# Performance work log

Hardware: AMD Instinct MI355X
Metric: run time of the kernel (lower is better)

## Reference

```python
import jax, jax.numpy as jnp
import numpy as np
import math

B, C, H, W = 4, 256, 64, 64
E = 96  # embed_dim
SOFTMAX_SCALE = 10.0
RESIDUAL_SCALE_INIT = 0.1


def conv1x1(w, x):
    # w: [out_c, in_c], x: [b, in_c, h, w] -> [b, out_c, h, w]
    return jnp.einsum('oc,bchw->bohw', w, x)


def setup_inputs() -> dict:
    key = jax.random.key(0)
    ks = jax.random.split(key, 12)
    s = 0.02
    return {
        'x': jax.random.normal(ks[0], (B, C, H, W), jnp.float32),
        'mask': jax.random.uniform(ks[1], (B, 1, H, W), jnp.float32),
        'ln_gamma': jnp.ones((C,), jnp.float32),
        'ln_beta': jnp.zeros((C,), jnp.float32),
        'wq': jax.random.normal(ks[2], (E, C), jnp.float32) * s,
        'wk': jax.random.normal(ks[3], (E, C), jnp.float32) * s,
        'wv': jax.random.normal(ks[4], (C, C), jnp.float32) * s,
        'w_out': jax.random.normal(ks[5], (C, C), jnp.float32) * s,
        'w_qm': jax.random.normal(ks[6], (E, 1), jnp.float32) * s,
        'wd1': jax.random.normal(ks[7], (C, 2 * C), jnp.float32) * s,
        'wd2': jax.random.normal(ks[8], (C, C), jnp.float32) * s,
        'wg': jax.random.normal(ks[9], (C, C + 1), jnp.float32) * s,
        'residual_scale': jnp.asarray(RESIDUAL_SCALE_INIT, jnp.float32),
    }


def reference(x, mask, ln_gamma, ln_beta, wq, wk, wv, w_out, w_qm, wd1, wd2, wg,
              residual_scale):
    b, c, h, w = x.shape
    n = h * w

    # ChannelLayerNorm: LayerNorm over channel dim
    mu = jnp.mean(x, axis=1, keepdims=True)
    var = jnp.mean((x - mu) ** 2, axis=1, keepdims=True)
    x_norm = (x - mu) / jnp.sqrt(var + 1e-5)
    x_norm = x_norm * ln_gamma[None, :, None, None] + ln_beta[None, :, None, None]

    # Q/K/V projections (1x1 convs), flatten to [b, n, d]
    q = conv1x1(wq, x_norm) + conv1x1(w_qm, mask)
    q = q.reshape(b, E, n).transpose(0, 2, 1)        # [b, n, E]
    k = conv1x1(wk, x_norm).reshape(b, E, n).transpose(0, 2, 1)  # [b, n, E]
    v = conv1x1(wv, x).reshape(b, c, n).transpose(0, 2, 1)       # [b, n, C]

    # cosine normalization (F.normalize with eps=1e-12)
    q = q / jnp.clip(jnp.linalg.norm(q, axis=-1, keepdims=True), 1e-12)
    k = k / jnp.clip(jnp.linalg.norm(k, axis=-1, keepdims=True), 1e-12)

    scale = SOFTMAX_SCALE / math.sqrt(E)
    attn = jnp.einsum('bqe,bke->bqk', q, k) * scale  # [b, n, n]

    # keys with mask >= 0.5 are invalid -> bias -10000
    invalid_keys = (mask.reshape(b, 1, n) >= 0.5)    # [b, 1, n]
    attn = jnp.where(invalid_keys, jnp.float32(-10000.0), attn)
    attn = jax.nn.softmax(attn, axis=-1)

    attended = jnp.einsum('bqk,bkc->bqc', attn, v)   # [b, n, C]
    attended = attended.transpose(0, 2, 1).reshape(b, c, h, w)
    attended = conv1x1(w_out, attended)

    # delta correction branch
    corr_in = jnp.concatenate([attended - x, x_norm * mask], axis=1)  # [b, 2C, h, w]
    hidden = jax.nn.gelu(conv1x1(wd1, corr_in), approximate=False)
    corrective = conv1x1(wd2, hidden)

    # MaskConditionedGate (assumed): sigmoid(1x1 conv over [corrective, mask])
    gate_in = jnp.concatenate([corrective, mask], axis=1)  # [b, C+1, h, w]
    gate = jax.nn.sigmoid(conv1x1(wg, gate_in)) * mask

    delta = jnp.tanh(residual_scale) * gate * corrective
    return x + delta
```

## Files before the change

### kernel.cpp

```cpp
#include <hip/hip_runtime.h>
#include <hip/hip_bf16.h>
#include <math.h>

#define BB 4
#define CC 256
#define NN 4096
#define EE 96
#define NTOT (BB*NN)

typedef __attribute__((ext_vector_type(8))) short bf16x8;
typedef __attribute__((ext_vector_type(4))) float f32x4;

__device__ __forceinline__ short f2bf(float x) {
    __hip_bfloat16 h = __float2bfloat16(x);
    return *reinterpret_cast<short*>(&h);
}
__device__ __forceinline__ float bf2f(short s) {
    unsigned int u = ((unsigned int)(unsigned short)s) << 16;
    float f;
    __builtin_memcpy(&f, &u, 4);
    return f;
}
__device__ __forceinline__ float gelu_exact(float v) {
    return 0.5f * v * (1.0f + erff(v * 0.70710678118654752f));
}
__device__ __forceinline__ void gld16(void* lds, const void* g) {
    __builtin_amdgcn_global_load_lds(
        (const __attribute__((address_space(1))) unsigned int*)g,
        (__attribute__((address_space(3))) unsigned int*)lds, 16, 0, 0);
}

#define OFF_WQ  0
#define OFF_WK  24576
#define OFF_WV  49152
#define OFF_WO  114688
#define OFF_WD1 180224
#define OFF_WD2 311296
#define OFF_WG  376832
#define OFF_WGL 442368
#define W16_TOTAL 442624

__global__ void wconv_kernel(const float* __restrict__ wq, const float* __restrict__ wk,
                             const float* __restrict__ wv, const float* __restrict__ wo,
                             const float* __restrict__ wd1, const float* __restrict__ wd2,
                             const float* __restrict__ wg, short* __restrict__ W16) {
    int i = blockIdx.x * 256 + threadIdx.x;
    if (i >= W16_TOTAL) return;
    float v;
    if      (i < OFF_WK)  v = wq[i];
    else if (i < OFF_WV)  v = wk[i - OFF_WK];
    else if (i < OFF_WO)  v = wv[i - OFF_WV];
    else if (i < OFF_WD1) v = wo[i - OFF_WO];
    else if (i < OFF_WD2) v = wd1[i - OFF_WD1];
    else if (i < OFF_WG)  v = wd2[i - OFF_WD2];
    else if (i < OFF_WGL) { int l = i - OFF_WG; v = wg[(l >> 8) * 257 + (l & 255)]; }
    else                  v = wg[(i - OFF_WGL) * 257 + 256];
    W16[i] = f2bf(v);
}

__global__ __launch_bounds__(256) void ln_kernel(
    const float* __restrict__ x, const float* __restrict__ gamma,
    const float* __restrict__ beta,
    short* __restrict__ Xt16, short* __restrict__ Xn16) {
    __shared__ float tile[256 * 33];
    __shared__ float psum[8][32], psq[8][32];
    __shared__ float mu_s[32], rs_s[32];
    __shared__ float gs[256], bs[256];
    const int b  = blockIdx.x >> 7;
    const int p0 = (blockIdx.x & 127) * 32;
    const int tid = threadIdx.x;
    const float* xb = x + (size_t)b * CC * NN;

    gs[tid] = gamma[tid];
    bs[tid] = beta[tid];
    #pragma unroll
    for (int i = 0; i < 8; ++i) {
        int idx = tid + i * 256;
        int c = idx >> 3, p4 = (idx & 7) * 4;
        float4 v = *(const float4*)&xb[(size_t)c * NN + p0 + p4];
        tile[c * 33 + p4]     = v.x;
        tile[c * 33 + p4 + 1] = v.y;
        tile[c * 33 + p4 + 2] = v.z;
        tile[c * 33 + p4 + 3] = v.w;
    }
    __syncthreads();
    {
        int col = tid & 31, part = tid >> 5;
        float s = 0.f, sq = 0.f;
        for (int r = part * 32; r < part * 32 + 32; ++r) {
            float v = tile[r * 33 + col];
            s += v; sq += v * v;
        }
        psum[part][col] = s; psq[part][col] = sq;
    }
    __syncthreads();
    if (tid < 32) {
        float S = 0.f, SQ = 0.f;
        #pragma unroll
        for (int j = 0; j < 8; ++j) { S += psum[j][tid]; SQ += psq[j][tid]; }
        float mu = S / 256.0f;
        float var = SQ / 256.0f - mu * mu;
        mu_s[tid] = mu;
        rs_s[tid] = rsqrtf(var + 1e-5f);
    }
    __syncthreads();
    size_t rowbase = ((size_t)b * NN + p0) * CC;
    #pragma unroll
    for (int i = 0; i < 4; ++i) {
        int idx = tid + i * 256;
        int p = idx >> 5, c8 = (idx & 31) * 8;
        float mu = mu_s[p], rcp = rs_s[p];
        bf16x8 xt, xn;
        #pragma unroll
        for (int j = 0; j < 8; ++j) {
            float v = tile[(c8 + j) * 33 + p];
            float n = (v - mu) * rcp * gs[c8 + j] + bs[c8 + j];
            xt[j] = f2bf(v); xn[j] = f2bf(n);
        }
        size_t o = rowbase + (size_t)p * CC + c8;
        *(bf16x8*)&Xt16[o] = xt;
        *(bf16x8*)&Xn16[o] = xn;
    }
}

__global__ __launch_bounds__(256) void qkproj_kernel(
    const short* __restrict__ Xn16, const short* __restrict__ W16,
    const float* __restrict__ mask, const float* __restrict__ w_qm,
    short* __restrict__ Q16, short* __restrict__ K16)
{
    const int tid = threadIdx.x;
    const int w = tid >> 6, lane = tid & 63, ln = lane & 15, quad = lane >> 4;
    const int m0 = blockIdx.x * 32 + (w & 1) * 16;
    const bool isQ = (w < 2);
    const int woff = isQ ? OFF_WQ : OFF_WK;

    f32x4 acc[6];
    #pragma unroll
    for (int i = 0; i < 6; ++i) acc[i] = (f32x4){0.f, 0.f, 0.f, 0.f};

    #pragma unroll
    for (int kt = 0; kt < 8; ++kt) {
        bf16x8 af = *(const bf16x8*)&Xn16[(size_t)(m0 + ln) * 256 + kt * 32 + quad * 8];
        #pragma unroll
        for (int nt = 0; nt < 6; ++nt) {
            bf16x8 bf = *(const bf16x8*)&W16[woff + (size_t)(nt * 16 + ln) * 256 + kt * 32 + quad * 8];
            acc[nt] = __builtin_amdgcn_mfma_f32_16x16x32_bf16(af, bf, acc[nt], 0, 0, 0);
        }
    }

    short* outp = isQ ? Q16 : K16;
    #pragma unroll
    for (int r = 0; r < 4; ++r) {
        int row = m0 + quad * 4 + r;
        float mrow = isQ ? mask[row] : 0.f;
        float vals[6];
        float ss = 0.f;
        #pragma unroll
        for (int nt = 0; nt < 6; ++nt) {
            float v = acc[nt][r];
            if (isQ) v += mrow * w_qm[nt * 16 + ln];
            vals[nt] = v;
            ss += v * v;
        }
        ss += __shfl_xor(ss, 1, 64); ss += __shfl_xor(ss, 2, 64);
        ss += __shfl_xor(ss, 4, 64); ss += __shfl_xor(ss, 8, 64);
        float sc = 1.0f / fmaxf(sqrtf(ss), 1e-12f);
        #pragma unroll
        for (int nt = 0; nt < 6; ++nt)
            outp[(size_t)row * EE + nt * 16 + ln] = f2bf(vals[nt] * sc);
    }
}

__global__ __launch_bounds__(256) void vproj_kernel(
    const short* __restrict__ Xt16, const short* __restrict__ W16,
    short* __restrict__ V16t)
{
    __shared__ short Vt[256 * 40];
    const int tid = threadIdx.x;
    const int w = tid >> 6, lane = tid & 63, ln = lane & 15, quad = lane >> 4;
    const int m0 = blockIdx.x * 32;
    const int wm = w >> 1, wn = w & 1;
    const int mrow = m0 + wm * 16;

    f32x4 acc[8];
    #pragma unroll
    for (int i = 0; i < 8; ++i) acc[i] = (f32x4){0.f, 0.f, 0.f, 0.f};

    #pragma unroll
    for (int kt = 0; kt < 8; ++kt) {
        bf16x8 af = *(const bf16x8*)&Xt16[(size_t)(mrow + ln) * 256 + kt * 32 + quad * 8];
        #pragma unroll
        for (int nt = 0; nt < 8; ++nt) {
            int col = wn * 128 + nt * 16 + ln;
            bf16x8 bf = *(const bf16x8*)&W16[OFF_WV + (size_t)col * 256 + kt * 32 + quad * 8];
            acc[nt] = __builtin_amdgcn_mfma_f32_16x16x32_bf16(af, bf, acc[nt], 0, 0, 0);
        }
    }
    #pragma unroll
    for (int nt = 0; nt < 8; ++nt) {
        int ch = wn * 128 + nt * 16 + ln;
        #pragma unroll
        for (int r = 0; r < 4; ++r)
            Vt[ch * 40 + wm * 16 + quad * 4 + r] = f2bf(acc[nt][r]);
    }
    __syncthreads();
    const int b = m0 >> 12, p0l = m0 & 4095;
    #pragma unroll
    for (int i = 0; i < 4; ++i) {
        int idx = tid + i * 256;
        int ch = idx >> 2, p8 = (idx & 3) * 8;
        *(bf16x8*)&V16t[((size_t)b * CC + ch) * NN + p0l + p8] =
            *(const bf16x8*)&Vt[ch * 40 + p8];
    }
}

__global__ __launch_bounds__(256, 4) void attn_kernel(
    const short* __restrict__ Q16, const short* __restrict__ K16,
    const short* __restrict__ V16t, const float* __restrict__ mask,
    short* __restrict__ Opart, float* __restrict__ Lpart)
{
    __shared__ short Vs[8192];
    __shared__ short Ks[3072];
    __shared__ short Ps[64 * 40];
    __shared__ float flg[32];

    const int tid = threadIdx.x;
    const int w = tid >> 6, lane = tid & 63, ln = lane & 15, quad = lane >> 4;
    const int bidx = blockIdx.x;
    const int kg = bidx >> 8;
    const int qg = bidx & 255;
    const int b  = (qg & 7) >> 1;
    const int qt = ((qg >> 3) << 1) | (qg & 1);
    const int q0 = qt * 64;
    const size_t bN = (size_t)b * NN;
    const size_t bCC = (size_t)b * CC;
    const int kbase = kg * 1024;
    const float C1 = 1.02062072615966f;
    const int wbase = w * 64;

    bf16x8 qf[3];
    #pragma unroll
    for (int e = 0; e < 3; ++e)
        qf[e] = *(const bf16x8*)&Q16[(bN + q0 + w * 16 + ln) * EE + e * 32 + quad * 8];

    f32x4 acc[4][4];
    #pragma unroll
    for (int mt = 0; mt < 4; ++mt)
        #pragma unroll
        for (int nt = 0; nt < 4; ++nt) acc[mt][nt] = (f32x4){0.f, 0.f, 0.f, 0.f};
    float lsum[4] = {0.f, 0.f, 0.f, 0.f};

    gld16(&Ks[wbase * 8], &K16[(bN + kbase + (tid & 31)) * EE + (tid >> 5) * 8]);
    if (w < 2)
        gld16(&Ks[(256 + wbase) * 8],
              &K16[(bN + kbase + (tid & 31)) * EE + (8 + (tid >> 5)) * 8]);
    if (w == 3 && lane < 8)
        gld16(&flg[0], &mask[bN + kbase + lane * 4]);
    __syncthreads();

    for (int it = 0; it < 32; ++it) {
        const int k0 = kbase + it * 32;
        #pragma unroll
        for (int i = 0; i < 4; ++i)
            gld16(&Vs[(i * 256 + wbase) * 8], &V16t[(bCC + tid) * NN + k0 + i * 8]);

        f32x4 s0 = (f32x4){0.f,0.f,0.f,0.f}, s1 = s0;
        #pragma unroll
        for (int e = 0; e < 3; ++e) {
            bf16x8 kf0 = *(const bf16x8*)&Ks[((e * 4 + quad) * 32 + ln) * 8];
            bf16x8 kf1 = *(const bf16x8*)&Ks[((e * 4 + quad) * 32 + 16 + ln) * 8];
            s0 = __builtin_amdgcn_mfma_f32_16x16x32_bf16(qf[e], kf0, s0, 0, 0, 0);
            s1 = __builtin_amdgcn_mfma_f32_16x16x32_bf16(qf[e], kf1, s1, 0, 0, 0);
        }
        bool z0 = flg[ln] >= 0.5f;
        bool z1 = flg[16 + ln] >= 0.5f;
        #pragma unroll
        for (int r = 0; r < 4; ++r) {
            float p0 = z0 ? 0.f : __expf(fmaf(s0[r], C1, -C1));
            float p1 = z1 ? 0.f : __expf(fmaf(s1[r], C1, -C1));
            lsum[r] += p0 + p1;
            Ps[(w * 16 + quad * 4 + r) * 40 + ln]      = f2bf(p0);
            Ps[(w * 16 + quad * 4 + r) * 40 + 16 + ln] = f2bf(p1);
        }
        __syncthreads();

        if (it + 1 < 32) {
            const int k0n = k0 + 32;
            gld16(&Ks[wbase * 8], &K16[(bN + k0n + (tid & 31)) * EE + (tid >> 5) * 8]);
            if (w < 2)
                gld16(&Ks[(256 + wbase) * 8],
                      &K16[(bN + k0n + (tid & 31)) * EE + (8 + (tid >> 5)) * 8]);
            if (w == 3 && lane < 8)
                gld16(&flg[0], &mask[bN + k0n + lane * 4]);
        }

        #pragma unroll
        for (int mt = 0; mt < 4; ++mt) {
            bf16x8 pf = *(const bf16x8*)&Ps[(mt * 16 + ln) * 40 + quad * 8];
            #pragma unroll
            for (int nt = 0; nt < 4; ++nt) {
                bf16x8 vf = *(const bf16x8*)&Vs[(quad * 256 + wbase + nt * 16 + ln) * 8];
                acc[mt][nt] = __builtin_amdgcn_mfma_f32_16x16x32_bf16(pf, vf, acc[mt][nt], 0, 0, 0);
            }
        }
        __syncthreads();
    }

    #pragma unroll
    for (int r = 0; r < 4; ++r) {
        float l = lsum[r];
        l += __shfl_xor(l, 1, 64); l += __shfl_xor(l, 2, 64);
        l += __shfl_xor(l, 4, 64); l += __shfl_xor(l, 8, 64);
        if (ln == 0)
            Lpart[(size_t)kg * NTOT + bN + q0 + w * 16 + quad * 4 + r] = l;
    }
    #pragma unroll
    for (int mt = 0; mt < 4; ++mt)
        #pragma unroll
        for (int nt = 0; nt < 4; ++nt)
            #pragma unroll
            for (int r = 0; r < 4; ++r)
                Opart[((size_t)kg * NTOT + bN + q0 + mt * 16 + quad * 4 + r) * 256
                      + wbase + nt * 16 + ln] = f2bf(acc[mt][nt][r]);
}

__global__ __launch_bounds__(256, 2) void epi_kernel(
    const short* __restrict__ Opart, const float* __restrict__ Lpart,
    const short* __restrict__ W16, const short* __restrict__ Xt16,
    const short* __restrict__ Xn16, const float* __restrict__ mask,
    const float* __restrict__ rs, const float* __restrict__ x,
    float* __restrict__ out)
{
    __shared__ char lds[54400];
    short* Olds  = (short*)lds;
    short* Hlds  = (short*)lds;
    short* Dlds  = (short*)(lds + 16896);
    short* Clds  = (short*)(lds + 16896);
    short* tileB = (short*)(lds + 33792);
    float* lsh   = (float*)(lds + 54272);

    const int tid = threadIdx.x;
    const int w = tid >> 6, lane = tid & 63, ln = lane & 15, quad = lane >> 4;
    const int wm = w >> 1, wn = w & 1;
    const int m0 = blockIdx.x * 32;
    const int b = m0 >> 12, p0l = m0 & 4095;

    if (tid < 32) {
        int g = m0 + tid;
        lsh[tid] = 1.0f / (Lpart[g] + Lpart[NTOT + g] + Lpart[2 * NTOT + g] + Lpart[3 * NTOT + g]);
    }
    __syncthreads();

    #pragma unroll
    for (int i = 0; i < 4; ++i) {
        int idx = tid + i * 256;
        int q = idx >> 5, ch8 = (idx & 31) * 8;
        size_t base = (size_t)(m0 + q) * 256 + ch8;
        bf16x8 a0 = *(const bf16x8*)&Opart[base];
        bf16x8 a1 = *(const bf16x8*)&Opart[(size_t)NTOT * 256 + base];
        bf16x8 a2 = *(const bf16x8*)&Opart[(size_t)2 * NTOT * 256 + base];
        bf16x8 a3 = *(const bf16x8*)&Opart[(size_t)3 * NTOT * 256 + base];
        float linv = lsh[q];
        bf16x8 o;
        #pragma unroll
        for (int e = 0; e < 8; ++e)
            o[e] = f2bf((bf2f(a0[e]) + bf2f(a1[e]) + bf2f(a2[e]) + bf2f(a3[e])) * linv);
        *(bf16x8*)&Olds[q * 264 + ch8] = o;
        bf16x8 xn = *(const bf16x8*)&Xn16[base];
        float mq = mask[m0 + q];
        bf16x8 xm;
        #pragma unroll
        for (int e = 0; e < 8; ++e) xm[e] = f2bf(bf2f(xn[e]) * mq);
        *(bf16x8*)&Dlds[q * 528 + 256 + ch8] = xm;
    }
    __syncthreads();

    {
        f32x4 acc[8];
        #pragma unroll
        for (int i = 0; i < 8; ++i) acc[i] = (f32x4){0.f, 0.f, 0.f, 0.f};
        #pragma unroll
        for (int kt = 0; kt < 8; ++kt) {
            bf16x8 af = *(const bf16x8*)&Olds[(wm * 16 + ln) * 264 + kt * 32 + quad * 8];
            #pragma unroll
            for (int nt = 0; nt < 8; ++nt) {
                int col = wn * 128 + nt * 16 + ln;
                bf16x8 bf = *(const bf16x8*)&W16[OFF_WO + (size_t)col * 256 + kt * 32 + quad * 8];
                acc[nt] = __builtin_amdgcn_mfma_f32_16x16x32_bf16(af, bf, acc[nt], 0, 0, 0);
            }
        }
        #pragma unroll
        for (int nt = 0; nt < 8; ++nt) {
            int col = wn * 128 + nt * 16 + ln;
            #pragma unroll
            for (int r = 0; r < 4; ++r) {
                int row = wm * 16 + quad * 4 + r;
                float v = acc[nt][r] - bf2f(Xt16[(size_t)(m0 + row) * 256 + col]);
                Dlds[row * 528 + col] = f2bf(v);
            }
        }
    }
    __syncthreads();

    {
        f32x4 acc[8];
        #pragma unroll
        for (int i = 0; i < 8; ++i) acc[i] = (f32x4){0.f, 0.f, 0.f, 0.f};
        #pragma unroll
        for (int kt = 0; kt < 16; ++kt) {
            bf16x8 af = *(const bf16x8*)&Dlds[(wm * 16 + ln) * 528 + kt * 32 + quad * 8];
            #pragma unroll
            for (int nt = 0; nt < 8; ++nt) {
                int col = wn * 128 + nt * 16 + ln;
                bf16x8 bf = *(const bf16x8*)&W16[OFF_WD1 + (size_t)col * 512 + kt * 32 + quad * 8];
                acc[nt] = __builtin_amdgcn_mfma_f32_16x16x32_bf16(af, bf, acc[nt], 0, 0, 0);
            }
        }
        __syncthreads();
        #pragma unroll
        for (int nt = 0; nt < 8; ++nt) {
            int col = wn * 128 + nt * 16 + ln;
            #pragma unroll
            for (int r = 0; r < 4; ++r) {
                int row = wm * 16 + quad * 4 + r;
                Hlds[row * 264 + col] = f2bf(gelu_exact(acc[nt][r]));
            }
        }
    }
    __syncthreads();

    {
        f32x4 acc[8];
        #pragma unroll
        for (int i = 0; i < 8; ++i) acc[i] = (f32x4){0.f, 0.f, 0.f, 0.f};
        #pragma unroll
        for (int kt = 0; kt < 8; ++kt) {
            bf16x8 af = *(const bf16x8*)&Hlds[(wm * 16 + ln) * 264 + kt * 32 + quad * 8];
            #pragma unroll
            for (int nt = 0; nt < 8; ++nt) {
                int col = wn * 128 + nt * 16 + ln;
                bf16x8 bf = *(const bf16x8*)&W16[OFF_WD2 + (size_t)col * 256 + kt * 32 + quad * 8];
                acc[nt] = __builtin_amdgcn_mfma_f32_16x16x32_bf16(af, bf, acc[nt], 0, 0, 0);
            }
        }
        __syncthreads();
        #pragma unroll
        for (int nt = 0; nt < 8; ++nt) {
            int col = wn * 128 + nt * 16 + ln;
            #pragma unroll
            for (int r = 0; r < 4; ++r) {
                int row = wm * 16 + quad * 4 + r;
                Clds[row * 264 + col] = f2bf(acc[nt][r]);
            }
        }
    }
    __syncthreads();

    {
        f32x4 acc[8];
        #pragma unroll
        for (int i = 0; i < 8; ++i) acc[i] = (f32x4){0.f, 0.f, 0.f, 0.f};
        #pragma unroll
        for (int kt = 0; kt < 8; ++kt) {
            bf16x8 af = *(const bf16x8*)&Clds[(wm * 16 + ln) * 264 + kt * 32 + quad * 8];
            #pragma unroll
            for (int nt = 0; nt < 8; ++nt) {
                int col = wn * 128 + nt * 16 + ln;
                bf16x8 bf = *(const bf16x8*)&W16[OFF_WG + (size_t)col * 256 + kt * 32 + quad * 8];
                acc[nt] = __builtin_amdgcn_mfma_f32_16x16x32_bf16(af, bf, acc[nt], 0, 0, 0);
            }
        }
        float trs = tanhf(rs[0]);
        #pragma unroll
        for (int nt = 0; nt < 8; ++nt) {
            int col = wn * 128 + nt * 16 + ln;
            float wgl = bf2f(W16[OFF_WGL + col]);
            #pragma unroll
            for (int r = 0; r < 4; ++r) {
                int row = wm * 16 + quad * 4 + r;
                float mrow = mask[m0 + row];
                float logit = acc[nt][r] + mrow * wgl;
                float gate = mrow / (1.0f + __expf(-logit));
                float corr = bf2f(Clds[row * 264 + col]);
                tileB[col * 40 + row] = f2bf(trs * gate * corr);
            }
        }
    }
    __syncthreads();

    #pragma unroll
    for (int i = 0; i < 4; ++i) {
        int idx = tid + i * 256;
        int ch = idx >> 2, p8 = (idx & 3) * 8;
        bf16x8 d = *(const bf16x8*)&tileB[ch * 40 + p8];
        size_t o = ((size_t)b * CC + ch) * NN + p0l + p8;
        float4 x0 = *(const float4*)&x[o];
        float4 x1 = *(const float4*)&x[o + 4];
        float4 o0, o1;
        o0.x = x0.x + bf2f(d[0]); o0.y = x0.y + bf2f(d[1]);
        o0.z = x0.z + bf2f(d[2]); o0.w = x0.w + bf2f(d[3]);
        o1.x = x1.x + bf2f(d[4]); o1.y = x1.y + bf2f(d[5]);
        o1.z = x1.z + bf2f(d[6]); o1.w = x1.w + bf2f(d[7]);
        *(float4*)&out[o] = o0;
        *(float4*)&out[o + 4] = o1;
    }
}

extern "C" void kernel_launch(void* const* d_in, const int* in_sizes, int n_in,
                              void* d_out, int out_size, void* d_ws, size_t ws_size,
                              hipStream_t stream) {
    const float* x     = (const float*)d_in[0];
    const float* mask  = (const float*)d_in[1];
    const float* gamma = (const float*)d_in[2];
    const float* beta  = (const float*)d_in[3];
    const float* wq    = (const float*)d_in[4];
    const float* wk    = (const float*)d_in[5];
    const float* wv    = (const float*)d_in[6];
    const float* w_out = (const float*)d_in[7];
    const float* w_qm  = (const float*)d_in[8];
    const float* wd1   = (const float*)d_in[9];
    const float* wd2   = (const float*)d_in[10];
    const float* wg    = (const float*)d_in[11];
    const float* rs    = (const float*)d_in[12];
    float* out = (float*)d_out;

    const size_t NC = (size_t)NTOT * CC;
    const size_t NE = (size_t)NTOT * EE;
    short* Xn16  = (short*)d_ws;
    short* Xt16  = Xn16 + NC;
    short* Q16   = Xt16 + NC;
    short* K16   = Q16 + NE;
    short* V16t  = K16 + NE;
    short* W16   = V16t + NC;
    short* Opart = W16 + W16_TOTAL;
    float* Lpart = (float*)(Opart + 4 * NC);

    wconv_kernel<<<(W16_TOTAL + 255) / 256, 256, 0, stream>>>(wq, wk, wv, w_out,
                                                              wd1, wd2, wg, W16);
    ln_kernel<<<512, 256, 0, stream>>>(x, gamma, beta, Xt16, Xn16);
    qkproj_kernel<<<512, 256, 0, stream>>>(Xn16, W16, mask, w_qm, Q16, K16);
    vproj_kernel<<<512, 256, 0, stream>>>(Xt16, W16, V16t);
    attn_kernel<<<1024, 256, 0, stream>>>(Q16, K16, V16t, mask, Opart, Lpart);
    epi_kernel<<<512, 256, 0, stream>>>(Opart, Lpart, W16, Xt16, Xn16, mask,
                                        rs, x, out);
}
```

Baseline: 309.9 us.

## Fuse weight conversion into LN, merge QKV projection, halve epilogue tiles

Folds the weight bf16 conversion into the layernorm kernel and merges the Q/K and V projection kernels into one launch, which removes two launches. LN, projection and epilogue blocks now cover 16 positions instead of 32, giving twice as many blocks, and the epilogue's occupancy hint rises from 2 to 4 blocks per SM. In attention, mask values are loaded straight from global memory instead of staged in LDS, P tiles are written as packed 32-bit pairs via lane shuffles, and P/V fragments are preloaded before the MFMA loop. Smaller tiles reload each weight fragment for fewer rows, so weight traffic per row goes up.

```diff
diff --git a/kernel.cpp b/kernel.cpp
--- a/kernel.cpp
+++ b/kernel.cpp
@@ -9,6 +9,7 @@
 #define NTOT (BB*NN)
 
 typedef __attribute__((ext_vector_type(8))) short bf16x8;
+typedef __attribute__((ext_vector_type(4))) short bf16x4;
 typedef __attribute__((ext_vector_type(4))) float f32x4;
 
 __device__ __forceinline__ short f2bf(float x) {
@@ -40,177 +41,175 @@
 #define OFF_WGL 442368
 #define W16_TOTAL 442624
 
-__global__ void wconv_kernel(const float* __restrict__ wq, const float* __restrict__ wk,
-                             const float* __restrict__ wv, const float* __restrict__ wo,
-                             const float* __restrict__ wd1, const float* __restrict__ wd2,
-                             const float* __restrict__ wg, short* __restrict__ W16) {
-    int i = blockIdx.x * 256 + threadIdx.x;
-    if (i >= W16_TOTAL) return;
-    float v;
-    if      (i < OFF_WK)  v = wq[i];
-    else if (i < OFF_WV)  v = wk[i - OFF_WK];
-    else if (i < OFF_WO)  v = wv[i - OFF_WV];
-    else if (i < OFF_WD1) v = wo[i - OFF_WO];
-    else if (i < OFF_WD2) v = wd1[i - OFF_WD1];
-    else if (i < OFF_WG)  v = wd2[i - OFF_WD2];
-    else if (i < OFF_WGL) { int l = i - OFF_WG; v = wg[(l >> 8) * 257 + (l & 255)]; }
-    else                  v = wg[(i - OFF_WGL) * 257 + 256];
-    W16[i] = f2bf(v);
-}
-
 __global__ __launch_bounds__(256) void ln_kernel(
     const float* __restrict__ x, const float* __restrict__ gamma,
     const float* __restrict__ beta,
-    short* __restrict__ Xt16, short* __restrict__ Xn16) {
-    __shared__ float tile[256 * 33];
-    __shared__ float psum[8][32], psq[8][32];
-    __shared__ float mu_s[32], rs_s[32];
+    const float* __restrict__ wq, const float* __restrict__ wk,
+    const float* __restrict__ wv, const float* __restrict__ wo,
+    const float* __restrict__ wd1, const float* __restrict__ wd2,
+    const float* __restrict__ wg, short* __restrict__ W16,
+    short* __restrict__ Xt16, short* __restrict__ Xn16)
+{
+    __shared__ float tile[256 * 17];
+    __shared__ float psum[16][16], psq[16][16];
+    __shared__ float mu_s[16], rs_s[16];
     __shared__ float gs[256], bs[256];
-    const int b  = blockIdx.x >> 7;
-    const int p0 = (blockIdx.x & 127) * 32;
     const int tid = threadIdx.x;
+    const int b  = blockIdx.x >> 8;
+    const int p0 = (blockIdx.x & 255) * 16;
+
+    {
+        int i0 = blockIdx.x * 256 + tid;
+        #pragma unroll
+        for (int j = 0; j < 2; ++j) {
+            int i = i0 + j * 262144;
+            if (i < W16_TOTAL) {
+                float v;
+                if      (i < OFF_WK)  v = wq[i];
+                else if (i < OFF_WV)  v = wk[i - OFF_WK];
+                else if (i < OFF_WO)  v = wv[i - OFF_WV];
+                else if (i < OFF_WD1) v = wo[i - OFF_WO];
+                else if (i < OFF_WD2) v = wd1[i - OFF_WD1];
+                else if (i < OFF_WG)  v = wd2[i - OFF_WD2];
+                else if (i < OFF_WGL) { int l = i - OFF_WG; v = wg[(l >> 8) * 257 + (l & 255)]; }
+                else                  v = wg[(i - OFF_WGL) * 257 + 256];
+                W16[i] = f2bf(v);
+            }
+        }
+    }
+
     const float* xb = x + (size_t)b * CC * NN;
-
     gs[tid] = gamma[tid];
     bs[tid] = beta[tid];
     #pragma unroll
-    for (int i = 0; i < 8; ++i) {
+    for (int i = 0; i < 4; ++i) {
         int idx = tid + i * 256;
-        int c = idx >> 3, p4 = (idx & 7) * 4;
+        int c = idx >> 2, p4 = (idx & 3) * 4;
         float4 v = *(const float4*)&xb[(size_t)c * NN + p0 + p4];
-        tile[c * 33 + p4]     = v.x;
-        tile[c * 33 + p4 + 1] = v.y;
-        tile[c * 33 + p4 + 2] = v.z;
-        tile[c * 33 + p4 + 3] = v.w;
-    }
-    __syncthreads();
-    {
-        int col = tid & 31, part = tid >> 5;
+        tile[c * 17 + p4]     = v.x;
+        tile[c * 17 + p4 + 1] = v.y;
+        tile[c * 17 + p4 + 2] = v.z;
+        tile[c * 17 + p4 + 3] = v.w;
+    }
+    __syncthreads();
+    {
+        int col = tid & 15, part = tid >> 4;
         float s = 0.f, sq = 0.f;
-        for (int r = part * 32; r < part * 32 + 32; ++r) {
-            float v = tile[r * 33 + col];
+        for (int r = part * 16; r < part * 16 + 16; ++r) {
+            float v = tile[r * 17 + col];
             s += v; sq += v * v;
         }
         psum[part][col] = s; psq[part][col] = sq;
     }
     __syncthreads();
-    if (tid < 32) {
+    if (tid < 16) {
         float S = 0.f, SQ = 0.f;
         #pragma unroll
-        for (int j = 0; j < 8; ++j) { S += psum[j][tid]; SQ += psq[j][tid]; }
+        for (int j = 0; j < 16; ++j) { S += psum[j][tid]; SQ += psq[j][tid]; }
         float mu = S / 256.0f;
         float var = SQ / 256.0f - mu * mu;
         mu_s[tid] = mu;
         rs_s[tid] = rsqrtf(var + 1e-5f);
     }
     __syncthreads();
-    size_t rowbase = ((size_t)b * NN + p0) * CC;
-    #pragma unroll
-    for (int i = 0; i < 4; ++i) {
-        int idx = tid + i * 256;
-        int p = idx >> 5, c8 = (idx & 31) * 8;
+    {
+        int p = tid >> 4, c16 = (tid & 15) * 16;
         float mu = mu_s[p], rcp = rs_s[p];
-        bf16x8 xt, xn;
+        size_t o = ((size_t)b * NN + p0 + p) * CC + c16;
+        bf16x8 xt0, xn0, xt1, xn1;
         #pragma unroll
         for (int j = 0; j < 8; ++j) {
-            float v = tile[(c8 + j) * 33 + p];
-            float n = (v - mu) * rcp * gs[c8 + j] + bs[c8 + j];
-            xt[j] = f2bf(v); xn[j] = f2bf(n);
-        }
-        size_t o = rowbase + (size_t)p * CC + c8;
-        *(bf16x8*)&Xt16[o] = xt;
-        *(bf16x8*)&Xn16[o] = xn;
-    }
-}
-
-__global__ __launch_bounds__(256) void qkproj_kernel(
-    const short* __restrict__ Xn16, const short* __restrict__ W16,
-    const float* __restrict__ mask, const float* __restrict__ w_qm,
-    short* __restrict__ Q16, short* __restrict__ K16)
+            float v = tile[(c16 + j) * 17 + p];
+            float n = (v - mu) * rcp * gs[c16 + j] + bs[c16 + j];
+            xt0[j] = f2bf(v); xn0[j] = f2bf(n);
+            float v2 = tile[(c16 + 8 + j) * 17 + p];
+            float n2 = (v2 - mu) * rcp * gs[c16 + 8 + j] + bs[c16 + 8 + j];
+            xt1[j] = f2bf(v2); xn1[j] = f2bf(n2);
+        }
+        *(bf16x8*)&Xt16[o]     = xt0;
+        *(bf16x8*)&Xn16[o]     = xn0;
+        *(bf16x8*)&Xt16[o + 8] = xt1;
+        *(bf16x8*)&Xn16[o + 8] = xn1;
+    }
+}
+
+__global__ __launch_bounds__(256) void proj_kernel(
+    const short* __restrict__ Xn16, const short* __restrict__ Xt16,
+    const short* __restrict__ W16, const float* __restrict__ mask,
+    const float* __restrict__ w_qm,
+    short* __restrict__ Q16, short* __restrict__ K16, short* __restrict__ V16t)
 {
+    __shared__ short Vt[256 * 24];
     const int tid = threadIdx.x;
     const int w = tid >> 6, lane = tid & 63, ln = lane & 15, quad = lane >> 4;
-    const int m0 = blockIdx.x * 32 + (w & 1) * 16;
-    const bool isQ = (w < 2);
-    const int woff = isQ ? OFF_WQ : OFF_WK;
-
-    f32x4 acc[6];
-    #pragma unroll
-    for (int i = 0; i < 6; ++i) acc[i] = (f32x4){0.f, 0.f, 0.f, 0.f};
-
-    #pragma unroll
-    for (int kt = 0; kt < 8; ++kt) {
-        bf16x8 af = *(const bf16x8*)&Xn16[(size_t)(m0 + ln) * 256 + kt * 32 + quad * 8];
-        #pragma unroll
-        for (int nt = 0; nt < 6; ++nt) {
-            bf16x8 bf = *(const bf16x8*)&W16[woff + (size_t)(nt * 16 + ln) * 256 + kt * 32 + quad * 8];
-            acc[nt] = __builtin_amdgcn_mfma_f32_16x16x32_bf16(af, bf, acc[nt], 0, 0, 0);
-        }
-    }
-
-    short* outp = isQ ? Q16 : K16;
-    #pragma unroll
-    for (int r = 0; r < 4; ++r) {
-        int row = m0 + quad * 4 + r;
-        float mrow = isQ ? mask[row] : 0.f;
-        float vals[6];
-        float ss = 0.f;
-        #pragma unroll
-        for (int nt = 0; nt < 6; ++nt) {
-            float v = acc[nt][r];
-            if (isQ) v += mrow * w_qm[nt * 16 + ln];
-            vals[nt] = v;
-            ss += v * v;
-        }
-        ss += __shfl_xor(ss, 1, 64); ss += __shfl_xor(ss, 2, 64);
-        ss += __shfl_xor(ss, 4, 64); ss += __shfl_xor(ss, 8, 64);
-        float sc = 1.0f / fmaxf(sqrtf(ss), 1e-12f);
-        #pragma unroll
-        for (int nt = 0; nt < 6; ++nt)
-            outp[(size_t)row * EE + nt * 16 + ln] = f2bf(vals[nt] * sc);
-    }
-}
-
-__global__ __launch_bounds__(256) void vproj_kernel(
-    const short* __restrict__ Xt16, const short* __restrict__ W16,
-    short* __restrict__ V16t)
-{
-    __shared__ short Vt[256 * 40];
-    const int tid = threadIdx.x;
-    const int w = tid >> 6, lane = tid & 63, ln = lane & 15, quad = lane >> 4;
-    const int m0 = blockIdx.x * 32;
-    const int wm = w >> 1, wn = w & 1;
-    const int mrow = m0 + wm * 16;
-
-    f32x4 acc[8];
-    #pragma unroll
-    for (int i = 0; i < 8; ++i) acc[i] = (f32x4){0.f, 0.f, 0.f, 0.f};
-
-    #pragma unroll
-    for (int kt = 0; kt < 8; ++kt) {
-        bf16x8 af = *(const bf16x8*)&Xt16[(size_t)(mrow + ln) * 256 + kt * 32 + quad * 8];
+    const int m0 = blockIdx.x * 16;
+
+    if (w < 2) {
+        const int woff = (w == 0) ? OFF_WQ : OFF_WK;
+        f32x4 acc[6];
+        #pragma unroll
+        for (int i = 0; i < 6; ++i) acc[i] = (f32x4){0.f, 0.f, 0.f, 0.f};
+        #pragma unroll
+        for (int kt = 0; kt < 8; ++kt) {
+            bf16x8 af = *(const bf16x8*)&Xn16[(size_t)(m0 + ln) * 256 + kt * 32 + quad * 8];
+            #pragma unroll
+            for (int nt = 0; nt < 6; ++nt) {
+                bf16x8 bf = *(const bf16x8*)&W16[woff + (size_t)(nt * 16 + ln) * 256 + kt * 32 + quad * 8];
+                acc[nt] = __builtin_amdgcn_mfma_f32_16x16x32_bf16(af, bf, acc[nt], 0, 0, 0);
+            }
+        }
+        short* outp = (w == 0) ? Q16 : K16;
+        #pragma unroll
+        for (int r = 0; r < 4; ++r) {
+            int row = m0 + quad * 4 + r;
+            float mrow = (w == 0) ? mask[row] : 0.f;
+            float vals[6];
+            float ss = 0.f;
+            #pragma unroll
+            for (int nt = 0; nt < 6; ++nt) {
+                float v = acc[nt][r];
+                if (w == 0) v += mrow * w_qm[nt * 16 + ln];
+                vals[nt] = v;
+                ss += v * v;
+            }
+            ss += __shfl_xor(ss, 1, 64); ss += __shfl_xor(ss, 2, 64);
+            ss += __shfl_xor(ss, 4, 64); ss += __shfl_xor(ss, 8, 64);
+            float sc = 1.0f / fmaxf(sqrtf(ss), 1e-12f);
+            #pragma unroll
+            for (int nt = 0; nt < 6; ++nt)
+                outp[(size_t)row * EE + nt * 16 + ln] = f2bf(vals[nt] * sc);
+        }
+    } else {
+        const int wn = w - 2;
+        f32x4 acc[8];
+        #pragma unroll
+        for (int i = 0; i < 8; ++i) acc[i] = (f32x4){0.f, 0.f, 0.f, 0.f};
+        #pragma unroll
+        for (int kt = 0; kt < 8; ++kt) {
+            bf16x8 af = *(const bf16x8*)&Xt16[(size_t)(m0 + ln) * 256 + kt * 32 + quad * 8];
+            #pragma unroll
+            for (int nt = 0; nt < 8; ++nt) {
+                int col = wn * 128 + nt * 16 + ln;
+                bf16x8 bf = *(const bf16x8*)&W16[OFF_WV + (size_t)col * 256 + kt * 32 + quad * 8];
+                acc[nt] = __builtin_amdgcn_mfma_f32_16x16x32_bf16(af, bf, acc[nt], 0, 0, 0);
+            }
+        }
         #pragma unroll
         for (int nt = 0; nt < 8; ++nt) {
-            int col = wn * 128 + nt * 16 + ln;
-            bf16x8 bf = *(const bf16x8*)&W16[OFF_WV + (size_t)col * 256 + kt * 32 + quad * 8];
-            acc[nt] = __builtin_amdgcn_mfma_f32_16x16x32_bf16(af, bf, acc[nt], 0, 0, 0);
-        }
-    }
-    #pragma unroll
-    for (int nt = 0; nt < 8; ++nt) {
-        int ch = wn * 128 + nt * 16 + ln;
-        #pragma unroll
-        for (int r = 0; r < 4; ++r)
-            Vt[ch * 40 + wm * 16 + quad * 4 + r] = f2bf(acc[nt][r]);
+            int ch = wn * 128 + nt * 16 + ln;
+            #pragma unroll
+            for (int r = 0; r < 4; ++r)
+                Vt[ch * 24 + quad * 4 + r] = f2bf(acc[nt][r]);
+        }
     }
     __syncthreads();
     const int b = m0 >> 12, p0l = m0 & 4095;
     #pragma unroll
-    for (int i = 0; i < 4; ++i) {
-        int idx = tid + i * 256;
-        int ch = idx >> 2, p8 = (idx & 3) * 8;
+    for (int j = 0; j < 2; ++j) {
+        int idx = tid + j * 256;
+        int ch = idx >> 1, p8 = (idx & 1) * 8;
         *(bf16x8*)&V16t[((size_t)b * CC + ch) * NN + p0l + p8] =
-            *(const bf16x8*)&Vt[ch * 40 + p8];
+            *(const bf16x8*)&Vt[ch * 24 + p8];
     }
 }
 
@@ -222,7 +221,6 @@
     __shared__ short Vs[8192];
     __shared__ short Ks[3072];
     __shared__ short Ps[64 * 40];
-    __shared__ float flg[32];
 
     const int tid = threadIdx.x;
     const int w = tid >> 6, lane = tid & 63, ln = lane & 15, quad = lane >> 4;
@@ -254,8 +252,6 @@
     if (w < 2)
         gld16(&Ks[(256 + wbase) * 8],
               &K16[(bN + kbase + (tid & 31)) * EE + (8 + (tid >> 5)) * 8]);
-    if (w == 3 && lane < 8)
-        gld16(&flg[0], &mask[bN + kbase + lane * 4]);
     __syncthreads();
 
     for (int it = 0; it < 32; ++it) {
@@ -263,6 +259,9 @@
         #pragma unroll
         for (int i = 0; i < 4; ++i)
             gld16(&Vs[(i * 256 + wbase) * 8], &V16t[(bCC + tid) * NN + k0 + i * 8]);
+
+        float mk0 = mask[bN + k0 + ln];
+        float mk1 = mask[bN + k0 + 16 + ln];
 
         f32x4 s0 = (f32x4){0.f,0.f,0.f,0.f}, s1 = s0;
         #pragma unroll
@@ -272,15 +271,22 @@
             s0 = __builtin_amdgcn_mfma_f32_16x16x32_bf16(qf[e], kf0, s0, 0, 0, 0);
             s1 = __builtin_amdgcn_mfma_f32_16x16x32_bf16(qf[e], kf1, s1, 0, 0, 0);
         }
-        bool z0 = flg[ln] >= 0.5f;
-        bool z1 = flg[16 + ln] >= 0.5f;
+        bool z0 = mk0 >= 0.5f;
+        bool z1 = mk1 >= 0.5f;
         #pragma unroll
         for (int r = 0; r < 4; ++r) {
             float p0 = z0 ? 0.f : __expf(fmaf(s0[r], C1, -C1));
             float p1 = z1 ? 0.f : __expf(fmaf(s1[r], C1, -C1));
             lsum[r] += p0 + p1;
-            Ps[(w * 16 + quad * 4 + r) * 40 + ln]      = f2bf(p0);
-            Ps[(w * 16 + quad * 4 + r) * 40 + 16 + ln] = f2bf(p1);
+            unsigned a0 = (unsigned short)f2bf(p0);
+            unsigned a1 = (unsigned short)f2bf(p1);
+            unsigned b0 = (unsigned)__shfl_xor((int)a0, 1, 64);
+            unsigned b1 = (unsigned)__shfl_xor((int)a1, 1, 64);
+            if (!(ln & 1)) {
+                int row = w * 16 + quad * 4 + r;
+                *(unsigned*)&Ps[row * 40 + ln]      = a0 | (b0 << 16);
+                *(unsigned*)&Ps[row * 40 + 16 + ln] = a1 | (b1 << 16);
+            }
         }
         __syncthreads();
 
@@ -290,19 +296,20 @@
             if (w < 2)
                 gld16(&Ks[(256 + wbase) * 8],
                       &K16[(bN + k0n + (tid & 31)) * EE + (8 + (tid >> 5)) * 8]);
-            if (w == 3 && lane < 8)
-                gld16(&flg[0], &mask[bN + k0n + lane * 4]);
-        }
-
-        #pragma unroll
-        for (int mt = 0; mt < 4; ++mt) {
-            bf16x8 pf = *(const bf16x8*)&Ps[(mt * 16 + ln) * 40 + quad * 8];
-            #pragma unroll
-            for (int nt = 0; nt < 4; ++nt) {
-                bf16x8 vf = *(const bf16x8*)&Vs[(quad * 256 + wbase + nt * 16 + ln) * 8];
-                acc[mt][nt] = __builtin_amdgcn_mfma_f32_16x16x32_bf16(pf, vf, acc[mt][nt], 0, 0, 0);
-            }
-        }
+        }
+
+        bf16x8 pf[4], vf[4];
+        #pragma unroll
+        for (int mt = 0; mt < 4; ++mt)
+            pf[mt] = *(const bf16x8*)&Ps[(mt * 16 + ln) * 40 + quad * 8];
+        #pragma unroll
+        for (int nt = 0; nt < 4; ++nt)
+            vf[nt] = *(const bf16x8*)&Vs[(quad * 256 + wbase + nt * 16 + ln) * 8];
+        #pragma unroll
+        for (int mt = 0; mt < 4; ++mt)
+            #pragma unroll
+            for (int nt = 0; nt < 4; ++nt)
+                acc[mt][nt] = __builtin_amdgcn_mfma_f32_16x16x32_bf16(pf[mt], vf[nt], acc[mt][nt], 0, 0, 0);
         __syncthreads();
     }
 
@@ -324,36 +331,35 @@
                       + wbase + nt * 16 + ln] = f2bf(acc[mt][nt][r]);
 }
 
-__global__ __launch_bounds__(256, 2) void epi_kernel(
+__global__ __launch_bounds__(256, 4) void epi_kernel(
     const short* __restrict__ Opart, const float* __restrict__ Lpart,
     const short* __restrict__ W16, const short* __restrict__ Xt16,
     const short* __restrict__ Xn16, const float* __restrict__ mask,
     const float* __restrict__ rs, const float* __restrict__ x,
     float* __restrict__ out)
 {
-    __shared__ char lds[54400];
+    __shared__ char lds[27264];
     short* Olds  = (short*)lds;
     short* Hlds  = (short*)lds;
-    short* Dlds  = (short*)(lds + 16896);
-    short* Clds  = (short*)(lds + 16896);
-    short* tileB = (short*)(lds + 33792);
-    float* lsh   = (float*)(lds + 54272);
+    short* Dlds  = (short*)(lds + 8448);
+    short* Clds  = (short*)(lds + 8448);
+    short* tileB = (short*)(lds + 16896);
+    float* lsh   = (float*)(lds + 27136);
 
     const int tid = threadIdx.x;
     const int w = tid >> 6, lane = tid & 63, ln = lane & 15, quad = lane >> 4;
-    const int wm = w >> 1, wn = w & 1;
-    const int m0 = blockIdx.x * 32;
+    const int m0 = blockIdx.x * 16;
     const int b = m0 >> 12, p0l = m0 & 4095;
 
-    if (tid < 32) {
+    if (tid < 16) {
         int g = m0 + tid;
         lsh[tid] = 1.0f / (Lpart[g] + Lpart[NTOT + g] + Lpart[2 * NTOT + g] + Lpart[3 * NTOT + g]);
     }
     __syncthreads();
 
     #pragma unroll
-    for (int i = 0; i < 4; ++i) {
-        int idx = tid + i * 256;
+    for (int j = 0; j < 2; ++j) {
+        int idx = tid + j * 256;
         int q = idx >> 5, ch8 = (idx & 31) * 8;
         size_t base = (size_t)(m0 + q) * 256 + ch8;
         bf16x8 a0 = *(const bf16x8*)&Opart[base];
@@ -376,25 +382,25 @@
     __syncthreads();
 
     {
-        f32x4 acc[8];
-        #pragma unroll
-        for (int i = 0; i < 8; ++i) acc[i] = (f32x4){0.f, 0.f, 0.f, 0.f};
+        f32x4 acc[4];
+        #pragma unroll
+        for (int i = 0; i < 4; ++i) acc[i] = (f32x4){0.f, 0.f, 0.f, 0.f};
         #pragma unroll
         for (int kt = 0; kt < 8; ++kt) {
-            bf16x8 af = *(const bf16x8*)&Olds[(wm * 16 + ln) * 264 + kt * 32 + quad * 8];
-            #pragma unroll
-            for (int nt = 0; nt < 8; ++nt) {
-                int col = wn * 128 + nt * 16 + ln;
+            bf16x8 af = *(const bf16x8*)&Olds[ln * 264 + kt * 32 + quad * 8];
+            #pragma unroll
+            for (int nt = 0; nt < 4; ++nt) {
+                int col = w * 64 + nt * 16 + ln;
                 bf16x8 bf = *(const bf16x8*)&W16[OFF_WO + (size_t)col * 256 + kt * 32 + quad * 8];
                 acc[nt] = __builtin_amdgcn_mfma_f32_16x16x32_bf16(af, bf, acc[nt], 0, 0, 0);
             }
         }
         #pragma unroll
-        for (int nt = 0; nt < 8; ++nt) {
-            int col = wn * 128 + nt * 16 + ln;
+        for (int nt = 0; nt < 4; ++nt) {
+            int col = w * 64 + nt * 16 + ln;
             #pragma unroll
             for (int r = 0; r < 4; ++r) {
-                int row = wm * 16 + quad * 4 + r;
+                int row = quad * 4 + r;
                 float v = acc[nt][r] - bf2f(Xt16[(size_t)(m0 + row) * 256 + col]);
                 Dlds[row * 528 + col] = f2bf(v);
             }
@@ -403,106 +409,97 @@
     __syncthreads();
 
     {
-        f32x4 acc[8];
-        #pragma unroll
-        for (int i = 0; i < 8; ++i) acc[i] = (f32x4){0.f, 0.f, 0.f, 0.f};
+        f32x4 acc[4];
+        #pragma unroll
+        for (int i = 0; i < 4; ++i) acc[i] = (f32x4){0.f, 0.f, 0.f, 0.f};
         #pragma unroll
         for (int kt = 0; kt < 16; ++kt) {
-            bf16x8 af = *(const bf16x8*)&Dlds[(wm * 16 + ln) * 528 + kt * 32 + quad * 8];
-            #pragma unroll
-            for (int nt = 0; nt < 8; ++nt) {
-                int col = wn * 128 + nt * 16 + ln;
+            bf16x8 af = *(const bf16x8*)&Dlds[ln * 528 + kt * 32 + quad * 8];
+            #pragma unroll
+            for (int nt = 0; nt < 4; ++nt) {
+                int col = w * 64 + nt * 16 + ln;
                 bf16x8 bf = *(const bf16x8*)&W16[OFF_WD1 + (size_t)col * 512 + kt * 32 + quad * 8];
                 acc[nt] = __builtin_amdgcn_mfma_f32_16x16x32_bf16(af, bf, acc[nt], 0, 0, 0);
             }
         }
-        __syncthreads();
-        #pragma unroll
-        for (int nt = 0; nt < 8; ++nt) {
-            int col = wn * 128 + nt * 16 + ln;
-            #pragma unroll
-            for (int r = 0; r < 4; ++r) {
-                int row = wm * 16 + quad * 4 + r;
-                Hlds[row * 264 + col] = f2bf(gelu_exact(acc[nt][r]));
-            }
-        }
-    }
-    __syncthreads();
-
-    {
-        f32x4 acc[8];
-        #pragma unroll
-        for (int i = 0; i < 8; ++i) acc[i] = (f32x4){0.f, 0.f, 0.f, 0.f};
+        #pragma unroll
+        for (int nt = 0; nt < 4; ++nt) {
+            int col = w * 64 + nt * 16 + ln;
+            #pragma unroll
+            for (int r = 0; r < 4; ++r)
+                Hlds[(quad * 4 + r) * 264 + col] = f2bf(gelu_exact(acc[nt][r]));
+        }
+    }
+    __syncthreads();
+
+    {
+        f32x4 acc[4];
+        #pragma unroll
+        for (int i = 0; i < 4; ++i) acc[i] = (f32x4){0.f, 0.f, 0.f, 0.f};
         #pragma unroll
         for (int kt = 0; kt < 8; ++kt) {
-            bf16x8 af = *(const bf16x8*)&Hlds[(wm * 16 + ln) * 264 + kt * 32 + quad * 8];
-            #pragma unroll
-            for (int nt = 0; nt < 8; ++nt) {
-                int col = wn * 128 + nt * 16 + ln;
+            bf16x8 af = *(const bf16x8*)&Hlds[ln * 264 + kt * 32 + quad * 8];
+            #pragma unroll
+            for (int nt = 0; nt < 4; ++nt) {
+                int col = w * 64 + nt * 16 + ln;
                 bf16x8 bf = *(const bf16x8*)&W16[OFF_WD2 + (size_t)col * 256 + kt * 32 + quad * 8];
                 acc[nt] = __builtin_amdgcn_mfma_f32_16x16x32_bf16(af, bf, acc[nt], 0, 0, 0);
             }
         }
-        __syncthreads();
-        #pragma unroll
-        for (int nt = 0; nt < 8; ++nt) {
-            int col = wn * 128 + nt * 16 + ln;
-            #pragma unroll
-            for (int r = 0; r < 4; ++r) {
-                int row = wm * 16 + quad * 4 + r;
-                Clds[row * 264 + col] = f2bf(acc[nt][r]);
-            }
-        }
-    }
-    __syncthreads();
-
-    {
-        f32x4 acc[8];
-        #pragma unroll
-        for (int i = 0; i < 8; ++i) acc[i] = (f32x4){0.f, 0.f, 0.f, 0.f};
+        #pragma unroll
+        for (int nt = 0; nt < 4; ++nt) {
+            int col = w * 64 + nt * 16 + ln;
+            #pragma unroll
+            for (int r = 0; r < 4; ++r)
+                Clds[(quad * 4 + r) * 264 + col] = f2bf(acc[nt][r]);
+        }
+    }
+    __syncthreads();
+
+    {
+        f32x4 acc[4];
+        #pragma unroll
+        for (int i = 0; i < 4; ++i) acc[i] = (f32x4){0.f, 0.f, 0.f, 0.f};
         #pragma unroll
         for (int kt = 0; kt < 8; ++kt) {
-            bf16x8 af = *(const bf16x8*)&Clds[(wm * 16 + ln) * 264 + kt * 32 + quad * 8];
-            #pragma unroll
-            for (int nt = 0; nt < 8; ++nt) {
-                int col = wn * 128 + nt * 16 + ln;
+            bf16x8 af = *(const bf16x8*)&Clds[ln * 264 + kt * 32 + quad * 8];
+            #pragma unroll
+            for (int nt = 0; nt < 4; ++nt) {
+                int col = w * 64 + nt * 16 + ln;
                 bf16x8 bf = *(const bf16x8*)&W16[OFF_WG + (size_t)col * 256 + kt * 32 + quad * 8];
                 acc[nt] = __builtin_amdgcn_mfma_f32_16x16x32_bf16(af, bf, acc[nt], 0, 0, 0);
             }
         }
         float trs = tanhf(rs[0]);
         #pragma unroll
-        for (int nt = 0; nt < 8; ++nt) {
-            int col = wn * 128 + nt * 16 + ln;
+        for (int nt = 0; nt < 4; ++nt) {
+            int col = w * 64 + nt * 16 + ln;
             float wgl = bf2f(W16[OFF_WGL + col]);
             #pragma unroll
             for (int r = 0; r < 4; ++r) {
-                int row = wm * 16 + quad * 4 + r;
+                int row = quad * 4 + r;
                 float mrow = mask[m0 + row];
                 float logit = acc[nt][r] + mrow * wgl;
                 float gate = mrow / (1.0f + __expf(-logit));
                 float corr = bf2f(Clds[row * 264 + col]);
-                tileB[col * 40 + row] = f2bf(trs * gate * corr);
-            }
-        }
-    }
-    __syncthreads();
-
-    #pragma unroll
-    for (int i = 0; i < 4; ++i) {
-        int idx = tid + i * 256;
-        int ch = idx >> 2, p8 = (idx & 3) * 8;
-        bf16x8 d = *(const bf16x8*)&tileB[ch * 40 + p8];
-        size_t o = ((size_t)b * CC + ch) * NN + p0l + p8;
-        float4 x0 = *(const float4*)&x[o];
-        float4 x1 = *(const float4*)&x[o + 4];
-        float4 o0, o1;
-        o0.x = x0.x + bf2f(d[0]); o0.y = x0.y + bf2f(d[1]);
-        o0.z = x0.z + bf2f(d[2]); o0.w = x0.w + bf2f(d[3]);
-        o1.x = x1.x + bf2f(d[4]); o1.y = x1.y + bf2f(d[5]);
-        o1.z = x1.z + bf2f(d[6]); o1.w = x1.w + bf2f(d[7]);
-        *(float4*)&out[o] = o0;
-        *(float4*)&out[o + 4] = o1;
+                tileB[col * 20 + row] = f2bf(trs * gate * corr);
+            }
+        }
+    }
+    __syncthreads();
+
+    {
+        int ch = tid;
+        size_t o = ((size_t)b * CC + ch) * NN + p0l;
+        #pragma unroll
+        for (int i = 0; i < 4; ++i) {
+            bf16x4 d = *(const bf16x4*)&tileB[ch * 20 + i * 4];
+            float4 xv = *(const float4*)&x[o + i * 4];
+            float4 ov;
+            ov.x = xv.x + bf2f(d[0]); ov.y = xv.y + bf2f(d[1]);
+            ov.z = xv.z + bf2f(d[2]); ov.w = xv.w + bf2f(d[3]);
+            *(float4*)&out[o + i * 4] = ov;
+        }
     }
 }
 
@@ -535,12 +532,11 @@
     short* Opart = W16 + W16_TOTAL;
     float* Lpart = (float*)(Opart + 4 * NC);
 
-    wconv_kernel<<<(W16_TOTAL + 255) / 256, 256, 0, stream>>>(wq, wk, wv, w_out,
-                                                              wd1, wd2, wg, W16);
-    ln_kernel<<<512, 256, 0, stream>>>(x, gamma, beta, Xt16, Xn16);
-    qkproj_kernel<<<512, 256, 0, stream>>>(Xn16, W16, mask, w_qm, Q16, K16);
-    vproj_kernel<<<512, 256, 0, stream>>>(Xt16, W16, V16t);
+    ln_kernel<<<1024, 256, 0, stream>>>(x, gamma, beta, wq, wk, wv, w_out,
+                                        wd1, wd2, wg, W16, Xt16, Xn16);
+    proj_kernel<<<1024, 256, 0, stream>>>(Xn16, Xt16, W16, mask, w_qm,
+                                          Q16, K16, V16t);
     attn_kernel<<<1024, 256, 0, stream>>>(Q16, K16, V16t, mask, Opart, Lpart);
-    epi_kernel<<<512, 256, 0, stream>>>(Opart, Lpart, W16, Xt16, Xn16, mask,
-                                        rs, x, out);
-}
+    epi_kernel<<<1024, 256, 0, stream>>>(Opart, Lpart, W16, Xt16, Xn16, mask,
+                                         rs, x, out);
+}
```

New measurement: 333.3 us. +7.6%, slower.
